# Kernel tuning notes

Measured on AMD Instinct MI355X. Metric: run time of the kernel, lower is better.

The kernel has to match this reference:

```python
import jax, jax.numpy as jnp
import numpy as np

B, C, H, W = 8, 64, 128, 128
OUT, K, PAD = 128, 9, 1  # 3x3 kernel -> K=9 taps


def setup_inputs() -> dict:
    key = jax.random.key(0)
    ks = jax.random.split(key, 6)
    x = jax.random.normal(ks[0], (B, C, H, W), dtype=jnp.float32)
    # trained-like params: small random offsets (std ~1-2 px) and mask logits
    w_offset = jax.random.normal(ks[1], (2 * K, C, 3, 3), dtype=jnp.float32) * 0.05
    b_offset = jax.random.normal(ks[2], (2 * K,), dtype=jnp.float32) * 0.1
    w_mask = jax.random.normal(ks[3], (K, C, 3, 3), dtype=jnp.float32) * 0.05
    b_mask = jax.random.normal(ks[4], (K,), dtype=jnp.float32) * 0.1
    w_conv = jax.random.normal(ks[5], (OUT, C, 3, 3), dtype=jnp.float32) * (1.0 / np.sqrt(C * 9))
    return {"x": x, "w_offset": w_offset, "b_offset": b_offset,
            "w_mask": w_mask, "b_mask": b_mask, "w_conv": w_conv}


def _conv3x3(x, w, b):
    out = jax.lax.conv_general_dilated(
        x, w, window_strides=(1, 1), padding=((PAD, PAD), (PAD, PAD)),
        dimension_numbers=("NCHW", "OIHW", "NCHW"))
    return out + b[None, :, None, None]


def _bilinear_gather(img, gy, gx):
    # img: [C,H,W]; gy,gx: [K,H,W] float sampling coords (zero outside bounds)
    C_, H_, W_ = img.shape
    y0 = jnp.floor(gy)
    x0 = jnp.floor(gx)
    wy = gy - y0
    wx = gx - x0
    img_flat = img.reshape(C_, H_ * W_)

    def corner(yi, xi, wgt):
        valid = ((yi >= 0) & (yi < H_) & (xi >= 0) & (xi < W_)).astype(img.dtype)
        yc = jnp.clip(yi, 0, H_ - 1).astype(jnp.int32)
        xc = jnp.clip(xi, 0, W_ - 1).astype(jnp.int32)
        v = img_flat[:, yc * W_ + xc]  # [C,K,H,W]
        return v * (wgt * valid)[None]

    return (corner(y0, x0, (1 - wy) * (1 - wx))
            + corner(y0, x0 + 1, (1 - wy) * wx)
            + corner(y0 + 1, x0, wy * (1 - wx))
            + corner(y0 + 1, x0 + 1, wy * wx))  # [C,K,H,W]


def reference(x, w_offset, b_offset, w_mask, b_mask, w_conv):
    offset = _conv3x3(x, w_offset, b_offset)                  # [B,18,H,W]
    mask = jax.nn.sigmoid(_conv3x3(x, w_mask, b_mask))        # [B,9,H,W]
    B_, C_, H_, W_ = x.shape
    # torchvision layout: channel 2k = dy, 2k+1 = dx for kernel tap k
    off = offset.reshape(B_, K, 2, H_, W_)
    dy, dx = off[:, :, 0], off[:, :, 1]                       # [B,K,H,W]
    ky, kx = jnp.meshgrid(jnp.arange(3, dtype=x.dtype),
                          jnp.arange(3, dtype=x.dtype), indexing="ij")
    gy = jnp.arange(H_, dtype=x.dtype)[None, None, :, None] - PAD + ky.reshape(1, K, 1, 1) + dy
    gx = jnp.arange(W_, dtype=x.dtype)[None, None, None, :] - PAD + kx.reshape(1, K, 1, 1) + dx
    sampled = jax.vmap(_bilinear_gather)(x, gy, gx)           # [B,C,K,H,W]
    sampled = sampled * mask[:, None]                         # modulated (DCNv2)
    out = jnp.einsum("bckhw,ock->bohw", sampled, w_conv.reshape(OUT, C_, K))
    return out
```

## Files before the change

kernel.cpp:

```cpp
#include <hip/hip_runtime.h>
#include <math.h>

#define Himg 128
#define Wimg 128
#define HW   16384
#define Cin  64
#define Kk   9
#define OUTC 128
#define Bsz  8

typedef __attribute__((ext_vector_type(8))) _Float16 half8;
typedef __attribute__((ext_vector_type(4))) float   floatx4;

#define SPL8(v) ((half8){(v),(v),(v),(v),(v),(v),(v),(v)})

__global__ __launch_bounds__(256) void prep(const float* __restrict__ x,
                                            const float* __restrict__ w_conv,
                                            const float* __restrict__ w_offset,
                                            const float* __restrict__ w_mask,
                                            _Float16* __restrict__ xt,
                                            _Float16* __restrict__ wpk_h,
                                            _Float16* __restrict__ wpk2) {
    __shared__ _Float16 tile[Cin][130];
    int t   = threadIdx.x;
    int bid = blockIdx.x;

    if (bid < 1024) {
        int b = bid >> 7;
        int h = bid & 127;
        const float* xb = x + (size_t)b * Cin * HW + (size_t)h * Wimg;
#pragma unroll
        for (int j = 0; j < 32; ++j) {
            int e = t + j * 256;
            int c = e >> 7;
            int w = e & 127;
            tile[c][w] = (_Float16)xb[(size_t)c * HW + w];
        }
        __syncthreads();
        unsigned* dst = (unsigned*)xt + ((size_t)b * HW + (size_t)h * Wimg) * 32;
#pragma unroll
        for (int j = 0; j < 16; ++j) {
            int d  = t + j * 256;
            int w  = d >> 5;
            int cp = d & 31;
            union { unsigned u; _Float16 hh[2]; } pk;
            pk.hh[0] = tile[2 * cp][w];
            pk.hh[1] = tile[2 * cp + 1][w];
            dst[d] = pk.u;
        }
        return;
    }

    if (bid < 1024 + 288) {
        int idx = (bid - 1024) * 256 + t;
        if (idx < Kk * Cin * OUTC) {
            int i    = idx & 7;
            int l    = (idx >> 3) & 63;
            int g    = idx >> 9;
            int mt   = g & 7;
            int ch   = g >> 3;
            int kq   = l >> 4;
            int ln16 = l & 15;
            int o    = mt * 16 + ln16;
            int kl   = kq * 8 + i;
            int c    = (ch & 1) * 32 + kl;
            int kt   = ch >> 1;
            wpk_h[idx] = (_Float16)w_conv[(o * Cin + c) * 9 + kt];
        }
        return;
    }

    {
        int idx = (bid - 1312) * 256 + t;
        if (idx < 18 * 32 * 32) {
            int i    = idx & 7;
            int l    = (idx >> 3) & 63;
            int g    = idx >> 9;
            int mt0  = g & 1;
            int ch   = g >> 1;
            int kq   = l >> 4;
            int ln16 = l & 15;
            int m    = mt0 * 16 + ln16;
            int kl   = kq * 8 + i;
            int c    = (ch & 1) * 32 + kl;
            int kt   = ch >> 1;
            float v = 0.0f;
            if (m < 18)      v = w_offset[(m * Cin + c) * 9 + kt];
            else if (m < 27) v = w_mask[((m - 18) * Cin + c) * 9 + kt];
            wpk2[idx] = (_Float16)v;
        }
    }
}

__global__ __launch_bounds__(256, 3) void deform_fused(
        const _Float16* __restrict__ xt, const _Float16* __restrict__ wpk_h,
        const _Float16* __restrict__ wpk2,
        const float* __restrict__ b_offset, const float* __restrict__ b_mask,
        float* __restrict__ out) {
    __shared__ union SMem {
        struct { _Float16 V0[2][64][40]; float P[32][66]; } p0;
        struct { _Float16 V[2][64][40]; } p1;
    } sm;

    int t    = threadIdx.x;
    int bid  = blockIdx.x;
    int b    = bid & 7;
    int pb   = bid >> 3;
    int pix0 = pb * 64;
    int h    = pix0 >> 7;
    int w0   = pix0 & 127;

    int lane = t & 63;
    int wv   = t >> 6;
    int q    = t >> 2;
    int c4   = t & 3;
    int kq   = lane >> 4;
    int ln16 = lane & 15;

    const _Float16* xtb  = xt + (size_t)b * HW * Cin;
    const half8* wsrc    = (const half8*)wpk_h;
    const half8* w2src   = (const half8*)wpk2;

    floatx4 acc2[2];
    acc2[0] = (floatx4){0.f, 0.f, 0.f, 0.f};
    acc2[1] = (floatx4){0.f, 0.f, 0.f, 0.f};
    int mt0 = wv & 1;
    int ntA = wv >> 1;

    half8 pvA, pvB, af;

#define LOADX0(chn, DST) { \
    const int ktn = (chn) >> 1, cgn = (chn) & 1; \
    int row = h + (ktn / 3) - 1; \
    int col = w0 + q + (ktn % 3) - 1; \
    bool okc = (row >= 0) && (row < Himg) && (col >= 0) && (col < Wimg); \
    if (okc) DST = *(const half8*)(xtb + ((size_t)(row * Wimg + col)) * Cin \
                                   + cgn * 32 + c4 * 8); \
    else     DST = SPL8((_Float16)0.0f); \
}

#define P0STEP(ch, PV) { \
    *(half8*)&sm.p0.V0[(ch) & 1][q][c4 * 8] = PV; \
    half8 afc = af; \
    if ((ch) < 16) LOADX0((ch) + 2, PV); \
    if ((ch) < 17) af = w2src[((size_t)((ch) + 1) * 2 + mt0) * 64 + lane]; \
    __syncthreads(); \
    half8 b0 = *(const half8*)&sm.p0.V0[(ch) & 1][ntA * 16 + ln16][kq * 8]; \
    half8 b1 = *(const half8*)&sm.p0.V0[(ch) & 1][(ntA + 2) * 16 + ln16][kq * 8]; \
    acc2[0] = __builtin_amdgcn_mfma_f32_16x16x32_f16(afc, b0, acc2[0], 0, 0, 0); \
    acc2[1] = __builtin_amdgcn_mfma_f32_16x16x32_f16(afc, b1, acc2[1], 0, 0, 0); \
}

    LOADX0(0, pvA)
    LOADX0(1, pvB)
    af = w2src[(size_t)mt0 * 64 + lane];

    P0STEP(0,  pvA) P0STEP(1,  pvB) P0STEP(2,  pvA) P0STEP(3,  pvB)
    P0STEP(4,  pvA) P0STEP(5,  pvB) P0STEP(6,  pvA) P0STEP(7,  pvB)
    P0STEP(8,  pvA) P0STEP(9,  pvB) P0STEP(10, pvA) P0STEP(11, pvB)
    P0STEP(12, pvA) P0STEP(13, pvB) P0STEP(14, pvA) P0STEP(15, pvB)
    P0STEP(16, pvA) P0STEP(17, pvB)

#pragma unroll
    for (int j = 0; j < 2; ++j) {
        int nt = ntA + 2 * j;
#pragma unroll
        for (int r = 0; r < 4; ++r)
            sm.p0.P[mt0 * 16 + kq * 4 + r][nt * 16 + ln16] = acc2[j][r];
    }
    __syncthreads();

    int      geomr[9];
    unsigned wab[9], wcd[9];
    {
        float fh = (float)h, fw = (float)(w0 + q);
#pragma unroll
        for (int k = 0; k < 9; ++k) {
            float dyv = sm.p0.P[2 * k][q]     + b_offset[2 * k];
            float dxv = sm.p0.P[2 * k + 1][q] + b_offset[2 * k + 1];
            float mz  = sm.p0.P[18 + k][q]    + b_mask[k];
            float mkv = 1.0f / (1.0f + expf(-mz));

            float gy  = fh + (float)(k / 3) - 1.0f + dyv;
            float gx  = fw + (float)(k % 3) - 1.0f + dxv;
            float y0f = floorf(gy), x0f = floorf(gx);
            int   y0  = (int)y0f,   x0 = (int)x0f;
            float wy  = gy - y0f,   wx = gx - x0f;
            int   y1  = y0 + 1,     x1 = x0 + 1;

            bool vy0 = (y0 >= 0) && (y0 < Himg);
            bool vy1 = (y1 >= 0) && (y1 < Himg);
            bool vx0 = (x0 >= 0) && (x0 < Wimg);
            bool vx1 = (x1 >= 0) && (x1 < Wimg);

            float w00 = (vy0 && vx0) ? (1.0f - wy) * (1.0f - wx) * mkv : 0.0f;
            float w01 = (vy0 && vx1) ? (1.0f - wy) * wx          * mkv : 0.0f;
            float w10 = (vy1 && vx0) ? wy          * (1.0f - wx) * mkv : 0.0f;
            float w11 = (vy1 && vx1) ? wy          * wx          * mkv : 0.0f;

            int y0c = min(max(y0, 0), Himg - 1), y1c = min(max(y1, 0), Himg - 1);
            int x0c = min(max(x0, 0), Wimg - 1), x1c = min(max(x1, 0), Wimg - 1);
            geomr[k] = (y0c * Wimg + x0c) | ((x1c - x0c) << 14) | ((y1c - y0c) << 15);
            union { unsigned u; _Float16 hh[2]; } pk;
            pk.hh[0] = (_Float16)w00; pk.hh[1] = (_Float16)w01; wab[k] = pk.u;
            pk.hh[0] = (_Float16)w10; pk.hh[1] = (_Float16)w11; wcd[k] = pk.u;
        }
    }

    floatx4 acc[2][4];
#pragma unroll
    for (int i = 0; i < 2; ++i)
#pragma unroll
        for (int j = 0; j < 4; ++j) acc[i][j] = (floatx4){0.f, 0.f, 0.f, 0.f};
    int m0 = wv * 32;

    half8 gA0, gA1, gA2, gA3, gB0, gB1, gB2, gB3, ar0, ar1;

#define LOADG(chn, D0, D1, D2, D3) { \
    int gg = geomr[(chn) >> 1]; \
    const _Float16* xc = xtb + (size_t)(gg & 0x3fff) * Cin \
                         + ((chn) & 1) * 32 + c4 * 8; \
    int ob = (gg & 0x4000) >> 8;    \
    int oc = (gg & 0x8000) >> 2;    \
    D0 = *(const half8*)(xc); \
    D1 = *(const half8*)(xc + ob); \
    D2 = *(const half8*)(xc + oc); \
    D3 = *(const half8*)(xc + oc + ob); \
}

#define P1STEP(ch, G0, G1, G2, G3) { \
    union { unsigned u; _Float16 hh[2]; } u1, u2; \
    u1.u = wab[(ch) >> 1];  u2.u = wcd[(ch) >> 1]; \
    half8 vv = G0 * SPL8(u1.hh[0]) + G1 * SPL8(u1.hh[1]) \
             + G2 * SPL8(u2.hh[0]) + G3 * SPL8(u2.hh[1]); \
    *(half8*)&sm.p1.V[(ch) & 1][q][c4 * 8] = vv; \
    half8 a0c = ar0, a1c = ar1; \
    if ((ch) < 16) LOADG((ch) + 2, G0, G1, G2, G3); \
    if ((ch) < 17) { \
        ar0 = wsrc[((size_t)((ch) + 1) * 8 + 2 * wv) * 64 + lane]; \
        ar1 = wsrc[((size_t)((ch) + 1) * 8 + 2 * wv + 1) * 64 + lane]; \
    } \
    __syncthreads(); \
    half8 bf0 = *(const half8*)&sm.p1.V[(ch) & 1][ 0 + ln16][kq * 8]; \
    half8 bf1 = *(const half8*)&sm.p1.V[(ch) & 1][16 + ln16][kq * 8]; \
    half8 bf2 = *(const half8*)&sm.p1.V[(ch) & 1][32 + ln16][kq * 8]; \
    half8 bf3 = *(const half8*)&sm.p1.V[(ch) & 1][48 + ln16][kq * 8]; \
    acc[0][0] = __builtin_amdgcn_mfma_f32_16x16x32_f16(a0c, bf0, acc[0][0], 0, 0, 0); \
    acc[1][0] = __builtin_amdgcn_mfma_f32_16x16x32_f16(a1c, bf0, acc[1][0], 0, 0, 0); \
    acc[0][1] = __builtin_amdgcn_mfma_f32_16x16x32_f16(a0c, bf1, acc[0][1], 0, 0, 0); \
    acc[1][1] = __builtin_amdgcn_mfma_f32_16x16x32_f16(a1c, bf1, acc[1][1], 0, 0, 0); \
    acc[0][2] = __builtin_amdgcn_mfma_f32_16x16x32_f16(a0c, bf2, acc[0][2], 0, 0, 0); \
    acc[1][2] = __builtin_amdgcn_mfma_f32_16x16x32_f16(a1c, bf2, acc[1][2], 0, 0, 0); \
    acc[0][3] = __builtin_amdgcn_mfma_f32_16x16x32_f16(a0c, bf3, acc[0][3], 0, 0, 0); \
    acc[1][3] = __builtin_amdgcn_mfma_f32_16x16x32_f16(a1c, bf3, acc[1][3], 0, 0, 0); \
}

    LOADG(0, gA0, gA1, gA2, gA3)
    LOADG(1, gB0, gB1, gB2, gB3)
    ar0 = wsrc[(size_t)(2 * wv) * 64 + lane];
    ar1 = wsrc[(size_t)(2 * wv + 1) * 64 + lane];
    __syncthreads();

    P1STEP(0,  gA0, gA1, gA2, gA3) P1STEP(1,  gB0, gB1, gB2, gB3)
    P1STEP(2,  gA0, gA1, gA2, gA3) P1STEP(3,  gB0, gB1, gB2, gB3)
    P1STEP(4,  gA0, gA1, gA2, gA3) P1STEP(5,  gB0, gB1, gB2, gB3)
    P1STEP(6,  gA0, gA1, gA2, gA3) P1STEP(7,  gB0, gB1, gB2, gB3)
    P1STEP(8,  gA0, gA1, gA2, gA3) P1STEP(9,  gB0, gB1, gB2, gB3)
    P1STEP(10, gA0, gA1, gA2, gA3) P1STEP(11, gB0, gB1, gB2, gB3)
    P1STEP(12, gA0, gA1, gA2, gA3) P1STEP(13, gB0, gB1, gB2, gB3)
    P1STEP(14, gA0, gA1, gA2, gA3) P1STEP(15, gB0, gB1, gB2, gB3)
    P1STEP(16, gA0, gA1, gA2, gA3) P1STEP(17, gB0, gB1, gB2, gB3)

#pragma unroll
    for (int mtl = 0; mtl < 2; ++mtl) {
#pragma unroll
        for (int nt = 0; nt < 4; ++nt) {
#pragma unroll
            for (int r = 0; r < 4; ++r) {
                int o  = m0 + mtl * 16 + kq * 4 + r;
                int px = nt * 16 + ln16;
                out[(size_t)(b * OUTC + o) * HW + pix0 + px] = acc[mtl][nt][r];
            }
        }
    }
}

extern "C" void kernel_launch(void* const* d_in, const int* in_sizes, int n_in,
                              void* d_out, int out_size, void* d_ws, size_t ws_size,
                              hipStream_t stream) {
    const float* x        = (const float*)d_in[0];
    const float* w_offset = (const float*)d_in[1];
    const float* b_offset = (const float*)d_in[2];
    const float* w_mask   = (const float*)d_in[3];
    const float* b_mask   = (const float*)d_in[4];
    const float* w_conv   = (const float*)d_in[5];
    float* out = (float*)d_out;

    _Float16* wpk_h = (_Float16*)d_ws;
    _Float16* wpk2  = wpk_h + 73728;
    _Float16* xtb   = wpk2 + 18432;

    prep<<<1384, 256, 0, stream>>>(x, w_conv, w_offset, w_mask, xtb, wpk_h, wpk2);
    deform_fused<<<2048, 256, 0, stream>>>(xtb, wpk_h, wpk2, b_offset, b_mask, out);
}
```

Baseline: 171.9 us.

## Make each wavefront own 16 pixels to remove block-wide barriers

```diff
diff --git a/kernel.cpp b/kernel.cpp
--- a/kernel.cpp
+++ b/kernel.cpp
@@ -97,10 +97,8 @@
         const _Float16* __restrict__ wpk2,
         const float* __restrict__ b_offset, const float* __restrict__ b_mask,
         float* __restrict__ out) {
-    __shared__ union SMem {
-        struct { _Float16 V0[2][64][40]; float P[32][66]; } p0;
-        struct { _Float16 V[2][64][40]; } p1;
-    } sm;
+    __shared__ _Float16 Vw[4][2][16][40];
+    __shared__ float    Pw[4][32][16];
 
     int t    = threadIdx.x;
     int bid  = blockIdx.x;
@@ -113,6 +111,7 @@
     int lane = t & 63;
     int wv   = t >> 6;
     int q    = t >> 2;
+    int qloc = (lane >> 2) & 15;
     int c4   = t & 3;
     int kq   = lane >> 4;
     int ln16 = lane & 15;
@@ -121,13 +120,10 @@
     const half8* wsrc    = (const half8*)wpk_h;
     const half8* w2src   = (const half8*)wpk2;
 
-    floatx4 acc2[2];
-    acc2[0] = (floatx4){0.f, 0.f, 0.f, 0.f};
-    acc2[1] = (floatx4){0.f, 0.f, 0.f, 0.f};
-    int mt0 = wv & 1;
-    int ntA = wv >> 1;
-
-    half8 pvA, pvB, af;
+    floatx4 acc2_0 = (floatx4){0.f, 0.f, 0.f, 0.f};
+    floatx4 acc2_1 = (floatx4){0.f, 0.f, 0.f, 0.f};
+
+    half8 pvA, pvB;
 
 #define LOADX0(chn, DST) { \
     const int ktn = (chn) >> 1, cgn = (chn) & 1; \
@@ -140,20 +136,17 @@
 }
 
 #define P0STEP(ch, PV) { \
-    *(half8*)&sm.p0.V0[(ch) & 1][q][c4 * 8] = PV; \
-    half8 afc = af; \
+    half8 af0 = w2src[((size_t)(ch) * 2 + 0) * 64 + lane]; \
+    half8 af1 = w2src[((size_t)(ch) * 2 + 1) * 64 + lane]; \
+    *(half8*)&Vw[wv][(ch) & 1][qloc][c4 * 8] = PV; \
     if ((ch) < 16) LOADX0((ch) + 2, PV); \
-    if ((ch) < 17) af = w2src[((size_t)((ch) + 1) * 2 + mt0) * 64 + lane]; \
-    __syncthreads(); \
-    half8 b0 = *(const half8*)&sm.p0.V0[(ch) & 1][ntA * 16 + ln16][kq * 8]; \
-    half8 b1 = *(const half8*)&sm.p0.V0[(ch) & 1][(ntA + 2) * 16 + ln16][kq * 8]; \
-    acc2[0] = __builtin_amdgcn_mfma_f32_16x16x32_f16(afc, b0, acc2[0], 0, 0, 0); \
-    acc2[1] = __builtin_amdgcn_mfma_f32_16x16x32_f16(afc, b1, acc2[1], 0, 0, 0); \
+    half8 bf = *(const half8*)&Vw[wv][(ch) & 1][ln16][kq * 8]; \
+    acc2_0 = __builtin_amdgcn_mfma_f32_16x16x32_f16(af0, bf, acc2_0, 0, 0, 0); \
+    acc2_1 = __builtin_amdgcn_mfma_f32_16x16x32_f16(af1, bf, acc2_1, 0, 0, 0); \
 }
 
     LOADX0(0, pvA)
     LOADX0(1, pvB)
-    af = w2src[(size_t)mt0 * 64 + lane];
 
     P0STEP(0,  pvA) P0STEP(1,  pvB) P0STEP(2,  pvA) P0STEP(3,  pvB)
     P0STEP(4,  pvA) P0STEP(5,  pvB) P0STEP(6,  pvA) P0STEP(7,  pvB)
@@ -162,13 +155,10 @@
     P0STEP(16, pvA) P0STEP(17, pvB)
 
 #pragma unroll
-    for (int j = 0; j < 2; ++j) {
-        int nt = ntA + 2 * j;
-#pragma unroll
-        for (int r = 0; r < 4; ++r)
-            sm.p0.P[mt0 * 16 + kq * 4 + r][nt * 16 + ln16] = acc2[j][r];
-    }
-    __syncthreads();
+    for (int r = 0; r < 4; ++r) {
+        Pw[wv][kq * 4 + r][ln16]      = acc2_0[r];
+        Pw[wv][16 + kq * 4 + r][ln16] = acc2_1[r];
+    }
 
     int      geomr[9];
     unsigned wab[9], wcd[9];
@@ -176,9 +166,9 @@
         float fh = (float)h, fw = (float)(w0 + q);
 #pragma unroll
         for (int k = 0; k < 9; ++k) {
-            float dyv = sm.p0.P[2 * k][q]     + b_offset[2 * k];
-            float dxv = sm.p0.P[2 * k + 1][q] + b_offset[2 * k + 1];
-            float mz  = sm.p0.P[18 + k][q]    + b_mask[k];
+            float dyv = Pw[wv][2 * k][qloc]     + b_offset[2 * k];
+            float dxv = Pw[wv][2 * k + 1][qloc] + b_offset[2 * k + 1];
+            float mz  = Pw[wv][18 + k][qloc]    + b_mask[k];
             float mkv = 1.0f / (1.0f + expf(-mz));
 
             float gy  = fh + (float)(k / 3) - 1.0f + dyv;
@@ -207,14 +197,11 @@
         }
     }
 
-    floatx4 acc[2][4];
-#pragma unroll
-    for (int i = 0; i < 2; ++i)
-#pragma unroll
-        for (int j = 0; j < 4; ++j) acc[i][j] = (floatx4){0.f, 0.f, 0.f, 0.f};
-    int m0 = wv * 32;
-
-    half8 gA0, gA1, gA2, gA3, gB0, gB1, gB2, gB3, ar0, ar1;
+    floatx4 acc[8];
+#pragma unroll
+    for (int i = 0; i < 8; ++i) acc[i] = (floatx4){0.f, 0.f, 0.f, 0.f};
+
+    half8 gA0, gA1, gA2, gA3, gB0, gB1, gB2, gB3;
 
 #define LOADG(chn, D0, D1, D2, D3) { \
     int gg = geomr[(chn) >> 1]; \
@@ -229,37 +216,34 @@
 }
 
 #define P1STEP(ch, G0, G1, G2, G3) { \
+     \
+    half8 ar0 = wsrc[((size_t)(ch) * 8 + 0) * 64 + lane]; \
+    half8 ar1 = wsrc[((size_t)(ch) * 8 + 1) * 64 + lane]; \
+    half8 ar2 = wsrc[((size_t)(ch) * 8 + 2) * 64 + lane]; \
+    half8 ar3 = wsrc[((size_t)(ch) * 8 + 3) * 64 + lane]; \
+    half8 ar4 = wsrc[((size_t)(ch) * 8 + 4) * 64 + lane]; \
+    half8 ar5 = wsrc[((size_t)(ch) * 8 + 5) * 64 + lane]; \
+    half8 ar6 = wsrc[((size_t)(ch) * 8 + 6) * 64 + lane]; \
+    half8 ar7 = wsrc[((size_t)(ch) * 8 + 7) * 64 + lane]; \
     union { unsigned u; _Float16 hh[2]; } u1, u2; \
     u1.u = wab[(ch) >> 1];  u2.u = wcd[(ch) >> 1]; \
     half8 vv = G0 * SPL8(u1.hh[0]) + G1 * SPL8(u1.hh[1]) \
              + G2 * SPL8(u2.hh[0]) + G3 * SPL8(u2.hh[1]); \
-    *(half8*)&sm.p1.V[(ch) & 1][q][c4 * 8] = vv; \
-    half8 a0c = ar0, a1c = ar1; \
+    *(half8*)&Vw[wv][(ch) & 1][qloc][c4 * 8] = vv; \
     if ((ch) < 16) LOADG((ch) + 2, G0, G1, G2, G3); \
-    if ((ch) < 17) { \
-        ar0 = wsrc[((size_t)((ch) + 1) * 8 + 2 * wv) * 64 + lane]; \
-        ar1 = wsrc[((size_t)((ch) + 1) * 8 + 2 * wv + 1) * 64 + lane]; \
-    } \
-    __syncthreads(); \
-    half8 bf0 = *(const half8*)&sm.p1.V[(ch) & 1][ 0 + ln16][kq * 8]; \
-    half8 bf1 = *(const half8*)&sm.p1.V[(ch) & 1][16 + ln16][kq * 8]; \
-    half8 bf2 = *(const half8*)&sm.p1.V[(ch) & 1][32 + ln16][kq * 8]; \
-    half8 bf3 = *(const half8*)&sm.p1.V[(ch) & 1][48 + ln16][kq * 8]; \
-    acc[0][0] = __builtin_amdgcn_mfma_f32_16x16x32_f16(a0c, bf0, acc[0][0], 0, 0, 0); \
-    acc[1][0] = __builtin_amdgcn_mfma_f32_16x16x32_f16(a1c, bf0, acc[1][0], 0, 0, 0); \
-    acc[0][1] = __builtin_amdgcn_mfma_f32_16x16x32_f16(a0c, bf1, acc[0][1], 0, 0, 0); \
-    acc[1][1] = __builtin_amdgcn_mfma_f32_16x16x32_f16(a1c, bf1, acc[1][1], 0, 0, 0); \
-    acc[0][2] = __builtin_amdgcn_mfma_f32_16x16x32_f16(a0c, bf2, acc[0][2], 0, 0, 0); \
-    acc[1][2] = __builtin_amdgcn_mfma_f32_16x16x32_f16(a1c, bf2, acc[1][2], 0, 0, 0); \
-    acc[0][3] = __builtin_amdgcn_mfma_f32_16x16x32_f16(a0c, bf3, acc[0][3], 0, 0, 0); \
-    acc[1][3] = __builtin_amdgcn_mfma_f32_16x16x32_f16(a1c, bf3, acc[1][3], 0, 0, 0); \
+    half8 bf = *(const half8*)&Vw[wv][(ch) & 1][ln16][kq * 8]; \
+    acc[0] = __builtin_amdgcn_mfma_f32_16x16x32_f16(ar0, bf, acc[0], 0, 0, 0); \
+    acc[1] = __builtin_amdgcn_mfma_f32_16x16x32_f16(ar1, bf, acc[1], 0, 0, 0); \
+    acc[2] = __builtin_amdgcn_mfma_f32_16x16x32_f16(ar2, bf, acc[2], 0, 0, 0); \
+    acc[3] = __builtin_amdgcn_mfma_f32_16x16x32_f16(ar3, bf, acc[3], 0, 0, 0); \
+    acc[4] = __builtin_amdgcn_mfma_f32_16x16x32_f16(ar4, bf, acc[4], 0, 0, 0); \
+    acc[5] = __builtin_amdgcn_mfma_f32_16x16x32_f16(ar5, bf, acc[5], 0, 0, 0); \
+    acc[6] = __builtin_amdgcn_mfma_f32_16x16x32_f16(ar6, bf, acc[6], 0, 0, 0); \
+    acc[7] = __builtin_amdgcn_mfma_f32_16x16x32_f16(ar7, bf, acc[7], 0, 0, 0); \
 }
 
     LOADG(0, gA0, gA1, gA2, gA3)
     LOADG(1, gB0, gB1, gB2, gB3)
-    ar0 = wsrc[(size_t)(2 * wv) * 64 + lane];
-    ar1 = wsrc[(size_t)(2 * wv + 1) * 64 + lane];
-    __syncthreads();
 
     P1STEP(0,  gA0, gA1, gA2, gA3) P1STEP(1,  gB0, gB1, gB2, gB3)
     P1STEP(2,  gA0, gA1, gA2, gA3) P1STEP(3,  gB0, gB1, gB2, gB3)
@@ -272,15 +256,11 @@
     P1STEP(16, gA0, gA1, gA2, gA3) P1STEP(17, gB0, gB1, gB2, gB3)
 
 #pragma unroll
-    for (int mtl = 0; mtl < 2; ++mtl) {
-#pragma unroll
-        for (int nt = 0; nt < 4; ++nt) {
-#pragma unroll
-            for (int r = 0; r < 4; ++r) {
-                int o  = m0 + mtl * 16 + kq * 4 + r;
-                int px = nt * 16 + ln16;
-                out[(size_t)(b * OUTC + o) * HW + pix0 + px] = acc[mtl][nt][r];
-            }
+    for (int mt = 0; mt < 8; ++mt) {
+#pragma unroll
+        for (int r = 0; r < 4; ++r) {
+            int o = mt * 16 + kq * 4 + r;
+            out[(size_t)(b * OUTC + o) * HW + pix0 + wv * 16 + ln16] = acc[mt][r];
         }
     }
 }
```

Measured after the change: 165.2 us. 3.9% less time.
